# Kernel tuning notes

Measured on AMD Instinct MI355X. Metric: run time of the kernel, lower is better.

Reference implementation:

```python
import jax, jax.numpy as jnp
import numpy as np

PNUM = 128
BATCH = 8192


def setup_inputs() -> dict:
    key = jax.random.key(0)
    k0, k1, k2 = jax.random.split(key, 3)
    return {
        "pred0": jax.random.normal(k0, (BATCH, PNUM, 2), dtype=jnp.float32),
        "pred1": jax.random.normal(k1, (BATCH, PNUM, 2), dtype=jnp.float32),
        "gt": jax.random.normal(k2, (BATCH, PNUM, 2), dtype=jnp.float32),
    }


def _smooth_l1(d):
    # F.smooth_l1_loss with default beta=1.0, reduction='none'
    a = jnp.abs(d)
    return jnp.where(a < 1.0, 0.5 * d * d, a - 0.5)


def _match_loss(pred, gt):
    # pred, gt: [B, pnum, 2]
    pnum = pred.shape[1]
    # cyclic index: idx[i, j] = (i + j) % pnum  (row i = gt rolled by i)
    idx = (jnp.arange(pnum)[:, None] + jnp.arange(pnum)[None, :]) % pnum
    gt_expand = gt[:, idx]                      # [B, pnum, pnum, 2]
    diff = pred[:, None, :, :] - gt_expand      # broadcast pred over shift dim i
    dis = _smooth_l1(diff).sum(-1).mean(axis=2)  # [B, pnum] mean over vertices j
    return jnp.min(dis, axis=1)                  # min over cyclic shift i -> [B]


def reference(pred0, pred1, gt):
    loss = _match_loss(pred0, gt).mean() + _match_loss(pred1, gt).mean()
    return loss / 2.0
```

## Files before the change

### kernel.cpp

```cpp
#include <hip/hip_runtime.h>
#include <stdint.h>

#define PNUM 128
#define BATCH 8192
#define WPB 4
#define GRID1 (BATCH / WPB)

typedef _Float16 h2 __attribute__((ext_vector_type(2)));
typedef _Float16 h4 __attribute__((ext_vector_type(4)));
typedef uint32_t u32;

__device__ __forceinline__ u32 cvt2u(float x, float y) {
    return __builtin_bit_cast(u32, __builtin_amdgcn_cvt_pkrtz(x, y));
}

__device__ __forceinline__ void unit(u32 p, u32 q, float& acc, u32 cOne, u32 cNegHalf) {
    u32 d, a, m, t;
    asm("v_pk_add_f16 %0, %1, %2 neg_lo:[0,1] neg_hi:[0,1]" : "=v"(d) : "v"(p), "v"(q));
    asm("v_and_b32 %0, 0x7fff7fff, %1" : "=v"(a) : "v"(d));
    asm("v_pk_min_f16 %0, %1, %2" : "=v"(m) : "v"(a), "v"(cOne));
    asm("v_pk_fma_f16 %0, %1, %2, %3" : "=v"(t) : "v"(m), "v"(cNegHalf), "v"(a));
    asm("v_dot2_f32_f16 %0, %1, %2, %0" : "+v"(acc) : "v"(m), "v"(t));
}

__global__ __launch_bounds__(64 * WPB, 6) void match_fused(
        const float* __restrict__ pred0,
        const float* __restrict__ pred1,
        const float* __restrict__ gt,
        float* __restrict__ out) {
    __shared__ __align__(16) _Float16 lds[WPB][1024];
    __shared__ float bsum[WPB];

    const int t = threadIdx.x;
    const int k = t & 63;
    const int w = __builtin_amdgcn_readfirstlane(t >> 6);
    const int b = blockIdx.x * WPB + w;

    _Float16* base = lds[w];
    uint2* ringU = (uint2*)base;
    uint2* q0s   = (uint2*)(base + 512);
    uint2* q1s   = (uint2*)(base + 768);

    const float4* gv4 = (const float4*)(gt    + (size_t)b * (PNUM * 2));
    const float4* p0v = (const float4*)(pred0 + (size_t)b * (PNUM * 2));
    const float4* p1v = (const float4*)(pred1 + (size_t)b * (PNUM * 2));
    {
        float4 g = gv4[k];
        uint2 gh = {cvt2u(g.x, g.y), cvt2u(g.z, g.w)};
        ringU[k] = gh; ringU[k + 64] = gh;
        float4 p = p0v[k];
        q0s[k] = (uint2){cvt2u(p.x, p.y), cvt2u(p.z, p.w)};
        p = p1v[k];
        q1s[k] = (uint2){cvt2u(p.x, p.y), cvt2u(p.z, p.w)};
    }

    const uint4* q0U = (const uint4*)(base + 512);
    const uint4* q1U = (const uint4*)(base + 768);

    u32 cOne = 0x3C003C00u;
    u32 cNegHalf = 0xB800B800u;

    uint2 W  = ringU[k];
    uint2 na = ringU[k + 1];
    uint2 nb = ringU[k + 2];
    uint4 P0 = q0U[0];
    uint4 P1 = q1U[0];

    float a00 = 0.f, a01 = 0.f, a10 = 0.f, a11 = 0.f;

#pragma unroll 8
    for (int hh = 0; hh < 32; ++hh) {
        const int hn = hh + 1;
        uint2 na_n = ringU[k + 2 * hn + 1];
        uint2 nb_n = ringU[k + 2 * hn + 2];
        uint4 P0_n = q0U[hn];
        uint4 P1_n = q1U[hn];

        unit(P0.x, W.x,  a00, cOne, cNegHalf);
        unit(P0.y, W.y,  a00, cOne, cNegHalf);
        unit(P0.z, na.x, a00, cOne, cNegHalf);
        unit(P0.w, na.y, a00, cOne, cNegHalf);
        unit(P0.x, W.y,  a01, cOne, cNegHalf);
        unit(P0.y, na.x, a01, cOne, cNegHalf);
        unit(P0.z, na.y, a01, cOne, cNegHalf);
        unit(P0.w, nb.x, a01, cOne, cNegHalf);
        unit(P1.x, W.x,  a10, cOne, cNegHalf);
        unit(P1.y, W.y,  a10, cOne, cNegHalf);
        unit(P1.z, na.x, a10, cOne, cNegHalf);
        unit(P1.w, na.y, a10, cOne, cNegHalf);
        unit(P1.x, W.y,  a11, cOne, cNegHalf);
        unit(P1.y, na.x, a11, cOne, cNegHalf);
        unit(P1.z, na.y, a11, cOne, cNegHalf);
        unit(P1.w, nb.x, a11, cOne, cNegHalf);

        W = nb; na = na_n; nb = nb_n; P0 = P0_n; P1 = P1_n;
    }

    float r0 = fminf(a00, a01);
    float r1 = fminf(a10, a11);
#pragma unroll
    for (int m = 32; m > 0; m >>= 1) {
        r0 = fminf(r0, __shfl_xor(r0, m, 64));
        r1 = fminf(r1, __shfl_xor(r1, m, 64));
    }

    if (k == 0) bsum[w] = r0 + r1;
    __syncthreads();
    if (t == 0) {
        float blockpart = bsum[0] + bsum[1] + bsum[2] + bsum[3];
        atomicAdd(out, blockpart * (1.0f / (2.0f * BATCH * PNUM)));
    }
}

extern "C" void kernel_launch(void* const* d_in, const int* in_sizes, int n_in,
                              void* d_out, int out_size, void* d_ws, size_t ws_size,
                              hipStream_t stream) {
    const float* pred0 = (const float*)d_in[0];
    const float* pred1 = (const float*)d_in[1];
    const float* gt    = (const float*)d_in[2];
    float* out = (float*)d_out;

    (void)hipMemsetAsync(out, 0, sizeof(float), stream);
    match_fused<<<GRID1, 64 * WPB, 0, stream>>>(pred0, pred1, gt, out);
}
```

Measured before the change: 113.2 us.

## Hand-pipeline LDS reads with inline asm triple buffering and explicit waitcnt

Replaces the compiler-scheduled inner loop with a manually software-pipelined loop. It issues ds_read_b64/b128 through inline asm into three rotating register buffers and uses explicit s_waitcnt lgkmcnt with sched barriers, so LDS latency overlaps the packed-fp16 compute. Launch bounds are raised from 6 to 8 waves to allow higher occupancy. The risks are register pressure, a rigid schedule the compiler cannot reorder, and correctness resting on hand-counted lgkmcnt values and byte offsets.

```diff
diff --git a/kernel.cpp b/kernel.cpp
--- a/kernel.cpp
+++ b/kernel.cpp
@@ -6,9 +6,9 @@
 #define WPB 4
 #define GRID1 (BATCH / WPB)
 
-typedef _Float16 h2 __attribute__((ext_vector_type(2)));
-typedef _Float16 h4 __attribute__((ext_vector_type(4)));
 typedef uint32_t u32;
+typedef uint32_t u32x2 __attribute__((ext_vector_type(2)));
+typedef uint32_t u32x4 __attribute__((ext_vector_type(4)));
 
 __device__ __forceinline__ u32 cvt2u(float x, float y) {
     return __builtin_bit_cast(u32, __builtin_amdgcn_cvt_pkrtz(x, y));
@@ -23,7 +23,33 @@
     asm("v_dot2_f32_f16 %0, %1, %2, %0" : "+v"(acc) : "v"(m), "v"(t));
 }
 
-__global__ __launch_bounds__(64 * WPB, 6) void match_fused(
+#define DSR64(dst, addr, OFF) \
+    asm volatile("ds_read_b64 %0, %1 offset:" OFF : "=v"(dst) : "v"(addr))
+#define DSR128(dst, addr, OFF) \
+    asm volatile("ds_read_b128 %0, %1 offset:" OFF : "=v"(dst) : "v"(addr))
+#define WAITLG(N) \
+    asm volatile("s_waitcnt lgkmcnt(" #N ")" ::: "memory"); \
+    __builtin_amdgcn_sched_barrier(0)
+
+#define COMPUTE(naC, nbC, q0C, q1C, Wv) \
+    unit(q0C[0], Wv[0],  a00, cOne, cNegHalf); \
+    unit(q0C[1], Wv[1],  a00, cOne, cNegHalf); \
+    unit(q0C[2], naC[0], a00, cOne, cNegHalf); \
+    unit(q0C[3], naC[1], a00, cOne, cNegHalf); \
+    unit(q0C[0], Wv[1],  a01, cOne, cNegHalf); \
+    unit(q0C[1], naC[0], a01, cOne, cNegHalf); \
+    unit(q0C[2], naC[1], a01, cOne, cNegHalf); \
+    unit(q0C[3], nbC[0], a01, cOne, cNegHalf); \
+    unit(q1C[0], Wv[0],  a10, cOne, cNegHalf); \
+    unit(q1C[1], Wv[1],  a10, cOne, cNegHalf); \
+    unit(q1C[2], naC[0], a10, cOne, cNegHalf); \
+    unit(q1C[3], naC[1], a10, cOne, cNegHalf); \
+    unit(q1C[0], Wv[1],  a11, cOne, cNegHalf); \
+    unit(q1C[1], naC[0], a11, cOne, cNegHalf); \
+    unit(q1C[2], naC[1], a11, cOne, cNegHalf); \
+    unit(q1C[3], nbC[0], a11, cOne, cNegHalf)
+
+__global__ __launch_bounds__(64 * WPB, 8) void match_fused(
         const float* __restrict__ pred0,
         const float* __restrict__ pred1,
         const float* __restrict__ gt,
@@ -54,47 +80,46 @@
         q1s[k] = (uint2){cvt2u(p.x, p.y), cvt2u(p.z, p.w)};
     }
 
-    const uint4* q0U = (const uint4*)(base + 512);
-    const uint4* q1U = (const uint4*)(base + 768);
+    u32 ldsb = (u32)(uintptr_t)base;
+    u32 gA = ldsb + (u32)(k * 8);
+    u32 pA = ldsb + 1024;
+
+    asm volatile("s_waitcnt lgkmcnt(0)" ::: "memory");
+    __builtin_amdgcn_sched_barrier(0);
 
     u32 cOne = 0x3C003C00u;
     u32 cNegHalf = 0xB800B800u;
 
-    uint2 W  = ringU[k];
-    uint2 na = ringU[k + 1];
-    uint2 nb = ringU[k + 2];
-    uint4 P0 = q0U[0];
-    uint4 P1 = q1U[0];
+    u32x2 na0, nb0, na1, nb1, na2, nb2;
+    u32x4 q0b0, q1b0, q0b1, q1b1, q0b2, q1b2;
+
+    DSR64(nb2, gA, "0");
+    DSR64(na0, gA, "8");   DSR64(nb0, gA, "16");
+    DSR128(q0b0, pA, "0"); DSR128(q1b0, pA, "512");
+    DSR64(na1, gA, "24");  DSR64(nb1, gA, "32");
+    DSR128(q0b1, pA, "16"); DSR128(q1b1, pA, "528");
 
     float a00 = 0.f, a01 = 0.f, a10 = 0.f, a11 = 0.f;
 
-#pragma unroll 8
-    for (int hh = 0; hh < 32; ++hh) {
-        const int hn = hh + 1;
-        uint2 na_n = ringU[k + 2 * hn + 1];
-        uint2 nb_n = ringU[k + 2 * hn + 2];
-        uint4 P0_n = q0U[hn];
-        uint4 P1_n = q1U[hn];
-
-        unit(P0.x, W.x,  a00, cOne, cNegHalf);
-        unit(P0.y, W.y,  a00, cOne, cNegHalf);
-        unit(P0.z, na.x, a00, cOne, cNegHalf);
-        unit(P0.w, na.y, a00, cOne, cNegHalf);
-        unit(P0.x, W.y,  a01, cOne, cNegHalf);
-        unit(P0.y, na.x, a01, cOne, cNegHalf);
-        unit(P0.z, na.y, a01, cOne, cNegHalf);
-        unit(P0.w, nb.x, a01, cOne, cNegHalf);
-        unit(P1.x, W.x,  a10, cOne, cNegHalf);
-        unit(P1.y, W.y,  a10, cOne, cNegHalf);
-        unit(P1.z, na.x, a10, cOne, cNegHalf);
-        unit(P1.w, na.y, a10, cOne, cNegHalf);
-        unit(P1.x, W.y,  a11, cOne, cNegHalf);
-        unit(P1.y, na.x, a11, cOne, cNegHalf);
-        unit(P1.z, na.y, a11, cOne, cNegHalf);
-        unit(P1.w, nb.x, a11, cOne, cNegHalf);
-
-        W = nb; na = na_n; nb = nb_n; P0 = P0_n; P1 = P1_n;
+    for (int bdy = 0; bdy < 10; ++bdy) {
+        WAITLG(4);
+        COMPUTE(na0, nb0, q0b0, q1b0, nb2);
+        DSR64(na2, gA, "40");  DSR64(nb2, gA, "48");
+        DSR128(q0b2, pA, "32"); DSR128(q1b2, pA, "544");
+        WAITLG(4);
+        COMPUTE(na1, nb1, q0b1, q1b1, nb0);
+        DSR64(na0, gA, "56");  DSR64(nb0, gA, "64");
+        DSR128(q0b0, pA, "48"); DSR128(q1b0, pA, "560");
+        WAITLG(4);
+        COMPUTE(na2, nb2, q0b2, q1b2, nb1);
+        DSR64(na1, gA, "72");  DSR64(nb1, gA, "80");
+        DSR128(q0b1, pA, "64"); DSR128(q1b1, pA, "576");
+        gA += 48; pA += 48;
     }
+    WAITLG(4);
+    COMPUTE(na0, nb0, q0b0, q1b0, nb2);
+    WAITLG(0);
+    COMPUTE(na1, nb1, q0b1, q1b1, nb0);
 
     float r0 = fminf(a00, a01);
     float r1 = fminf(a10, a11);
```

After: 113.4 us. About the same (+0.2%).
